# Kernel optimization log

Measured on AMD Instinct MI355X. Metric: run time of the kernel, lower is better.

Reference implementation:

```python
import jax, jax.numpy as jnp
import numpy as np

B, S, D, H = 2, 4096, 512, 8
HD = D // H

def setup_inputs() -> dict:
    key = jax.random.key(0)
    ks = jax.random.split(key, 9)
    s = 1.0 / np.sqrt(D)
    inp = {"x": jax.random.normal(ks[0], (B, S, D), dtype=jnp.float32)}
    names = ["Wq", "Wk", "Wv", "Wo"]
    for i, n in enumerate(names):
        inp[n] = jax.random.uniform(ks[1 + 2 * i], (D, D), jnp.float32, -s, s)
        inp["b" + n[1]] = jax.random.uniform(ks[2 + 2 * i], (D,), jnp.float32, -s, s)
    return inp


def reference(x, Wq, bq, Wk, bk, Wv, bv, Wo, bo):
    # projections (torch Linear: x @ W.T + b)
    def proj(W, b):
        return (x @ W.T + b).reshape(B, S, H, HD).transpose(0, 2, 1, 3)  # [B,H,S,HD]
    q = proj(Wq, bq)
    k = proj(Wk, bk)
    v = proj(Wv, bv)
    scores = jnp.einsum("bhqd,bhkd->bhqk", q, k) / np.sqrt(HD).astype(np.float32)
    attn = jax.nn.softmax(scores, axis=-1)
    out = jnp.einsum("bhqk,bhkd->bhqd", attn, v)
    out = out.transpose(0, 2, 1, 3).reshape(B, S, D)
    return out @ Wo.T + bo
```

## Files before the change

kernel.cpp:

```cpp
#include <hip/hip_runtime.h>
#include <hip/hip_bf16.h>

#define DEV __device__ __forceinline__

typedef float f32x4 __attribute__((ext_vector_type(4)));
typedef float f32x16 __attribute__((ext_vector_type(16)));
typedef __bf16 bf16x8 __attribute__((ext_vector_type(8)));
typedef unsigned short u16;
typedef unsigned short u16x8 __attribute__((ext_vector_type(8)));

DEV u16 f2bf(float f) {
    __bf16 h = (__bf16)f;
    return __builtin_bit_cast(u16, h);
}
DEV float bf2f(u16 u) {
    __bf16 h = __builtin_bit_cast(__bf16, u);
    return (float)h;
}

DEV f32x4 mfma16(bf16x8 a, bf16x8 b, f32x4 c) {
    return __builtin_amdgcn_mfma_f32_16x16x32_bf16(a, b, c, 0, 0, 0);
}
DEV f32x16 mfma32(bf16x8 a, bf16x8 b, f32x16 c) {
    return __builtin_amdgcn_mfma_f32_32x32x16_bf16(a, b, c, 0, 0, 0);
}

DEV unsigned cvtpk(float lo, float hi) {
    unsigned r;
    asm("v_cvt_pk_bf16_f32 %0, %1, %2" : "=v"(r) : "v"(lo), "v"(hi));
    return r;
}
DEV void pswap(unsigned& a, unsigned& b) {
    asm volatile("v_permlane32_swap_b32 %0, %1" : "+v"(a), "+v"(b));
}

DEV void gll16(const u16* g, u16* l) {
    __builtin_amdgcn_global_load_lds(
        (const __attribute__((address_space(1))) unsigned int*)g,
        (__attribute__((address_space(3))) unsigned int*)l,
        16, 0, 0);
}

DEV int kidx(int row, int col) { return row * 64 + (col ^ ((row & 7) << 3)); }
DEV int xidx(int row, int col) { return row * 32 + (col ^ ((row & 3) << 3)); }

__global__ __launch_bounds__(256) void cvt_kernel(
    const float* __restrict__ x, const float* __restrict__ wq,
    const float* __restrict__ wk, const float* __restrict__ wv,
    const float* __restrict__ wo,
    u16* __restrict__ xb, u16* __restrict__ wb)
{
    size_t e0 = ((size_t)blockIdx.x * 256 + threadIdx.x) * 8;
    const float* src; u16* dst; size_t off;
    if (e0 < 4194304) { src = x; dst = xb; off = e0; }
    else {
        size_t r = e0 - 4194304;
        int seg = (int)(r >> 18);
        src = (seg == 0) ? wq : (seg == 1) ? wk : (seg == 2) ? wv : wo;
        dst = wb + (size_t)seg * 262144;
        off = r & 262143;
    }
    f32x4 a = *(const f32x4*)(src + off);
    f32x4 b = *(const f32x4*)(src + off + 4);
    u16x8 o;
    #pragma unroll
    for (int i = 0; i < 4; ++i) { o[i] = f2bf(a[i]); o[i + 4] = f2bf(b[i]); }
    *(u16x8*)(dst + off) = o;
}

__global__ __launch_bounds__(256) void proj_qkv_kernel(
    const u16* __restrict__ xb, const u16* __restrict__ wb,
    const float* __restrict__ bq, const float* __restrict__ bk, const float* __restrict__ bv,
    u16* __restrict__ qo, u16* __restrict__ ko, u16* __restrict__ vo)
{
    __shared__ u16 Xs[2][128 * 32], Wsh[2][128 * 32];
    const int tid = threadIdx.x;
    const int m0 = blockIdx.x * 128, n0 = blockIdx.y * 128, z = blockIdx.z;
    const u16* W = wb + (size_t)z * 262144;
    const float* bias = (z == 0) ? bq : (z == 1) ? bk : bv;

    const int lane = tid & 63, wv = tid >> 6;
    const int g = lane >> 4, c = lane & 15;
    const int wr = wv >> 1, wcl = wv & 1;

    const int r0 = wv * 32 + (lane >> 2);
    const int csz = (((lane & 3) ^ ((lane >> 2) & 3)) << 3);
    const u16* xg0 = xb + (size_t)(m0 + r0) * 512 + csz;
    const u16* xg1 = xg0 + 16 * 512;
    const u16* wg0 = W + (size_t)(n0 + r0) * 512 + csz;
    const u16* wg1 = wg0 + 16 * 512;

    f32x4 acc[4][4] = {};

    gll16(xg0, &Xs[0][wv * 1024]);
    gll16(xg1, &Xs[0][wv * 1024 + 512]);
    gll16(wg0, &Wsh[0][wv * 1024]);
    gll16(wg1, &Wsh[0][wv * 1024 + 512]);

    for (int it = 0; it < 16; ++it) {
        const int p = it & 1;
        __syncthreads();
        if (it < 15) {
            const int kn = (it + 1) * 32;
            gll16(xg0 + kn, &Xs[p ^ 1][wv * 1024]);
            gll16(xg1 + kn, &Xs[p ^ 1][wv * 1024 + 512]);
            gll16(wg0 + kn, &Wsh[p ^ 1][wv * 1024]);
            gll16(wg1 + kn, &Wsh[p ^ 1][wv * 1024 + 512]);
        }

        bf16x8 af[4], bfr[4];
        #pragma unroll
        for (int mt = 0; mt < 4; ++mt)
            af[mt] = *(const bf16x8*)&Xs[p][xidx(wr * 64 + mt * 16 + c, g * 8)];
        #pragma unroll
        for (int nt = 0; nt < 4; ++nt)
            bfr[nt] = *(const bf16x8*)&Wsh[p][xidx(wcl * 64 + nt * 16 + c, g * 8)];

        if (z < 2) {
            #pragma unroll
            for (int mt = 0; mt < 4; ++mt)
                #pragma unroll
                for (int nt = 0; nt < 4; ++nt)
                    acc[mt][nt] = mfma16(af[mt], bfr[nt], acc[mt][nt]);
        } else {
            #pragma unroll
            for (int mt = 0; mt < 4; ++mt)
                #pragma unroll
                for (int nt = 0; nt < 4; ++nt)
                    acc[mt][nt] = mfma16(bfr[nt], af[mt], acc[mt][nt]);
        }
    }

    if (z < 2) {
        const float scale = (z == 0) ? 0.18033688011112042f : 1.0f;
        u16* outp = (z == 0) ? qo : ko;
        float bn[4];
        #pragma unroll
        for (int nt = 0; nt < 4; ++nt) bn[nt] = bias[n0 + wcl * 64 + nt * 16 + c];
        #pragma unroll
        for (int mt = 0; mt < 4; ++mt)
            #pragma unroll
            for (int r = 0; r < 4; ++r) {
                int mg = m0 + wr * 64 + mt * 16 + g * 4 + r;
                int b = mg >> 12, s = mg & 4095;
                #pragma unroll
                for (int nt = 0; nt < 4; ++nt) {
                    int ng = n0 + wcl * 64 + nt * 16 + c;
                    int h = ng >> 6, d = ng & 63;
                    outp[((size_t)(b * 8 + h) * 4096 + s) * 64 + d] =
                        f2bf((acc[mt][nt][r] + bn[nt]) * scale);
                }
            }
    } else {
        #pragma unroll
        for (int nt = 0; nt < 4; ++nt)
            #pragma unroll
            for (int r = 0; r < 4; ++r) {
                int ng = n0 + wcl * 64 + nt * 16 + g * 4 + r;
                int h = ng >> 6, d = ng & 63;
                float bnr = bias[ng];
                #pragma unroll
                for (int mt = 0; mt < 4; ++mt) {
                    int mg = m0 + wr * 64 + mt * 16 + c;
                    int b = mg >> 12, s = mg & 4095;
                    vo[((size_t)(b * 8 + h) * 64 + d) * 4096 + s] =
                        f2bf(acc[mt][nt][r] + bnr);
                }
            }
    }
}

__global__ __launch_bounds__(256, 4) void flash_attn_kernel(
    const u16* __restrict__ Q, const u16* __restrict__ K,
    const u16* __restrict__ Vt, u16* __restrict__ Opart, float* __restrict__ lbuf)
{
    __shared__ u16 Ks[2][64 * 64];
    __shared__ u16 Vs[2][64 * 64];

    const int tid = threadIdx.x;
    const int bh = blockIdx.y;
    const int q0 = blockIdx.x * 128;
    const int half = blockIdx.z;
    const int kvbase = half * 2048;
    const int lane = tid & 63, wv = tid >> 6;
    const int l31 = lane & 31, hi = lane >> 5;

    const u16* Qb = Q  + (size_t)bh * (4096 * 64);
    const u16* Kb = K  + (size_t)bh * (4096 * 64);
    const u16* Vb = Vt + (size_t)bh * (64 * 4096);

    u16x8 onesu;
    #pragma unroll
    for (int i = 0; i < 8; ++i) onesu[i] = 0x3F80;
    const bf16x8 ones = __builtin_bit_cast(bf16x8, onesu);

    const int qrow = q0 + wv * 32 + l31;
    bf16x8 qf[4];
    #pragma unroll
    for (int ds = 0; ds < 4; ++ds)
        qf[ds] = *(const bf16x8*)(Qb + (size_t)qrow * 64 + ds * 16 + hi * 8);

    f32x16 oA[2] = {};
    f32x16 oL = {};

    const int kr = wv * 16 + (lane >> 3);
    const int csz = (((lane & 7) ^ (lane >> 3)) << 3);
    const u16* kg0 = Kb + (size_t)(kvbase + kr) * 64 + csz;
    const u16* kg1 = kg0 + 8 * 64;
    const u16* vg0 = Vb + (size_t)kr * 4096 + kvbase + csz;
    const u16* vg1 = vg0 + 8 * 4096;

    gll16(kg0, &Ks[0][wv * 1024]);
    gll16(kg1, &Ks[0][wv * 1024 + 512]);
    gll16(vg0, &Vs[0][wv * 1024]);
    gll16(vg1, &Vs[0][wv * 1024 + 512]);

    for (int t = 0; t < 32; ++t) {
        const int p = t & 1;
        __syncthreads();
        if (t < 31) {
            const size_t ko = (size_t)(t + 1) * 4096;
            const size_t vofs = (size_t)(t + 1) * 64;
            gll16(kg0 + ko, &Ks[p ^ 1][wv * 1024]);
            gll16(kg1 + ko, &Ks[p ^ 1][wv * 1024 + 512]);
            gll16(vg0 + vofs, &Vs[p ^ 1][wv * 1024]);
            gll16(vg1 + vofs, &Vs[p ^ 1][wv * 1024 + 512]);
        }

        #pragma unroll
        for (int ct = 0; ct < 2; ++ct) {
            f32x16 sA = {};
            __builtin_amdgcn_s_setprio(1);
            #pragma unroll
            for (int ds = 0; ds < 4; ++ds) {
                bf16x8 kf = *(const bf16x8*)&Ks[p][kidx(ct * 32 + l31, ds * 16 + hi * 8)];
                sA = mfma32(kf, qf[ds], sA);
            }
            __builtin_amdgcn_s_setprio(0);

            float pv[16];
            #pragma unroll
            for (int r = 0; r < 16; ++r)
                pv[r] = __builtin_amdgcn_exp2f(sA[r]);

            unsigned a0 = cvtpk(pv[0],  pv[1]),  a1 = cvtpk(pv[2],  pv[3]);
            unsigned b0 = cvtpk(pv[4],  pv[5]),  b1 = cvtpk(pv[6],  pv[7]);
            pswap(a0, b0); pswap(a1, b1);
            uint4 w0; w0.x = a0; w0.y = a1; w0.z = b0; w0.w = b1;
            bf16x8 pfa = __builtin_bit_cast(bf16x8, w0);
            unsigned c0 = cvtpk(pv[8],  pv[9]),  c1 = cvtpk(pv[10], pv[11]);
            unsigned d0 = cvtpk(pv[12], pv[13]), d1 = cvtpk(pv[14], pv[15]);
            pswap(c0, d0); pswap(c1, d1);
            uint4 w1; w1.x = c0; w1.y = c1; w1.z = d0; w1.w = d1;
            bf16x8 pfb = __builtin_bit_cast(bf16x8, w1);

            __builtin_amdgcn_s_setprio(1);
            oL = mfma32(ones, pfa, oL);
            oL = mfma32(ones, pfb, oL);
            #pragma unroll
            for (int hf = 0; hf < 2; ++hf) {
                const int ks = 2 * ct + hf;
                const bf16x8 pfx = hf ? pfb : pfa;
                bf16x8 vf0 = *(const bf16x8*)&Vs[p][kidx(l31,      ks * 16 + hi * 8)];
                bf16x8 vf1 = *(const bf16x8*)&Vs[p][kidx(32 + l31, ks * 16 + hi * 8)];
                oA[0] = mfma32(vf0, pfx, oA[0]);
                oA[1] = mfma32(vf1, pfx, oA[1]);
            }
            __builtin_amdgcn_s_setprio(0);
        }
    }

    if (hi == 0)
        lbuf[(size_t)(half * 16 + bh) * 4096 + qrow] = oL[0];

    const int b = bh >> 3, h = bh & 7;
    u16* Ob = Opart + (size_t)half * 4194304 +
              ((size_t)(b * 4096 + qrow)) * 512 + h * 64;
    #pragma unroll
    for (int dt = 0; dt < 2; ++dt) {
        const f32x16 oa = dt ? oA[1] : oA[0];
        #pragma unroll
        for (int qd = 0; qd < 4; ++qd) {
            unsigned w0 = cvtpk(oa[qd * 4 + 0], oa[qd * 4 + 1]);
            unsigned w1 = cvtpk(oa[qd * 4 + 2], oa[qd * 4 + 3]);
            uint2 st; st.x = w0; st.y = w1;
            *(uint2*)(Ob + dt * 32 + qd * 8 + hi * 4) = st;
        }
    }
}

__global__ __launch_bounds__(256) void combine_kernel(
    const u16* __restrict__ Opart, const float* __restrict__ lbuf,
    u16* __restrict__ obuf)
{
    const size_t idx8 = ((size_t)blockIdx.x * 256 + threadIdx.x) * 8;
    const int m = (int)(idx8 >> 9);
    const int hd = (int)(idx8 & 511);
    const int b = m >> 12, s = m & 4095, h = hd >> 6;
    const int bh = b * 8 + h;
    const float la = lbuf[(size_t)bh * 4096 + s];
    const float lb = lbuf[(size_t)(16 + bh) * 4096 + s];
    const float inv = 1.0f / (la + lb);
    u16x8 a = *(const u16x8*)(Opart + idx8);
    u16x8 c = *(const u16x8*)(Opart + 4194304 + idx8);
    u16x8 o;
    #pragma unroll
    for (int i = 0; i < 8; ++i)
        o[i] = f2bf((bf2f(a[i]) + bf2f(c[i])) * inv);
    *(u16x8*)(obuf + idx8) = o;
}

__global__ __launch_bounds__(256) void out_proj_kernel(
    const u16* __restrict__ Ob, const u16* __restrict__ Wob,
    const float* __restrict__ bo, float* __restrict__ out)
{
    __shared__ u16 Xs[2][128 * 32], Wsh[2][128 * 32];
    const int tid = threadIdx.x;
    const int m0 = blockIdx.x * 128, n0 = blockIdx.y * 128;

    const int lane = tid & 63, wv = tid >> 6;
    const int g = lane >> 4, c = lane & 15;
    const int wr = wv >> 1, wcl = wv & 1;

    const int r0 = wv * 32 + (lane >> 2);
    const int csz = (((lane & 3) ^ ((lane >> 2) & 3)) << 3);
    const u16* xg0 = Ob + (size_t)(m0 + r0) * 512 + csz;
    const u16* xg1 = xg0 + 16 * 512;
    const u16* wg0 = Wob + (size_t)(n0 + r0) * 512 + csz;
    const u16* wg1 = wg0 + 16 * 512;

    f32x4 acc[4][4] = {};

    gll16(xg0, &Xs[0][wv * 1024]);
    gll16(xg1, &Xs[0][wv * 1024 + 512]);
    gll16(wg0, &Wsh[0][wv * 1024]);
    gll16(wg1, &Wsh[0][wv * 1024 + 512]);

    for (int it = 0; it < 16; ++it) {
        const int p = it & 1;
        __syncthreads();
        if (it < 15) {
            const int kn = (it + 1) * 32;
            gll16(xg0 + kn, &Xs[p ^ 1][wv * 1024]);
            gll16(xg1 + kn, &Xs[p ^ 1][wv * 1024 + 512]);
            gll16(wg0 + kn, &Wsh[p ^ 1][wv * 1024]);
            gll16(wg1 + kn, &Wsh[p ^ 1][wv * 1024 + 512]);
        }

        bf16x8 af[4], bfr[4];
        #pragma unroll
        for (int mt = 0; mt < 4; ++mt)
            af[mt] = *(const bf16x8*)&Xs[p][xidx(wr * 64 + mt * 16 + c, g * 8)];
        #pragma unroll
        for (int nt = 0; nt < 4; ++nt)
            bfr[nt] = *(const bf16x8*)&Wsh[p][xidx(wcl * 64 + nt * 16 + c, g * 8)];

        #pragma unroll
        for (int mt = 0; mt < 4; ++mt)
            #pragma unroll
            for (int nt = 0; nt < 4; ++nt)
                acc[mt][nt] = mfma16(bfr[nt], af[mt], acc[mt][nt]);
    }

    #pragma unroll
    for (int nt = 0; nt < 4; ++nt) {
        f32x4 bi = *(const f32x4*)&bo[n0 + wcl * 64 + nt * 16 + g * 4];
        #pragma unroll
        for (int mt = 0; mt < 4; ++mt) {
            int m = m0 + wr * 64 + mt * 16 + c;
            f32x4 v;
            #pragma unroll
            for (int r = 0; r < 4; ++r) v[r] = acc[mt][nt][r] + bi[r];
            *(f32x4*)&out[(size_t)m * 512 + n0 + wcl * 64 + nt * 16 + g * 4] = v;
        }
    }
}

extern "C" void kernel_launch(void* const* d_in, const int* in_sizes, int n_in,
                              void* d_out, int out_size, void* d_ws, size_t ws_size,
                              hipStream_t stream) {
    const float* x  = (const float*)d_in[0];
    const float* Wq = (const float*)d_in[1];
    const float* bq = (const float*)d_in[2];
    const float* Wk = (const float*)d_in[3];
    const float* bk = (const float*)d_in[4];
    const float* Wv = (const float*)d_in[5];
    const float* bv = (const float*)d_in[6];
    const float* Wo = (const float*)d_in[7];
    const float* bo = (const float*)d_in[8];
    float* out = (float*)d_out;

    const size_t NQKV = (size_t)2 * 8 * 4096 * 64;
    u16* qw = (u16*)d_ws;
    u16* kw = qw + NQKV;
    u16* vw = kw + NQKV;
    u16* wbuf = vw + NQKV;
    float* lbuf = (float*)(wbuf + 4 * 262144);
    u16* xbuf = (u16*)(lbuf + 2 * 16 * 4096);
    u16* opart = (u16*)d_out;
    u16* obuf = qw;

    cvt_kernel<<<2560, 256, 0, stream>>>(x, Wq, Wk, Wv, Wo, xbuf, wbuf);
    proj_qkv_kernel<<<dim3(64, 4, 3), 256, 0, stream>>>(xbuf, wbuf, bq, bk, bv, qw, kw, vw);
    flash_attn_kernel<<<dim3(32, 16, 2), 256, 0, stream>>>(qw, kw, vw, opart, lbuf);
    combine_kernel<<<2048, 256, 0, stream>>>(opart, lbuf, obuf);
    out_proj_kernel<<<dim3(64, 4), 256, 0, stream>>>(obuf, wbuf + 3 * 262144, bo, out);
}
```

Measured before the change: 140.2 us.

## Split KV within block across waves and merge in LDS, dropping combine kernel

The flash attention kernel now processes 64 query rows per block, with two wave pairs each handling half of every 64-key tile, instead of splitting the KV range across two grid blocks. The partial outputs and row sums are merged through shared memory at the end, and the result is written normalized directly. This removes the separate combine kernel and the bf16 partial-output round trip through global memory. In exchange each wave does half the compute per tile, so per-tile sync and load overhead is amortized over less math, and there is an extra LDS exchange at the end.

Result: no change. 140.5 us (+0.2%).

```diff
diff --git a/kernel.cpp b/kernel.cpp
--- a/kernel.cpp
+++ b/kernel.cpp
@@ -12,10 +12,6 @@
 DEV u16 f2bf(float f) {
     __bf16 h = (__bf16)f;
     return __builtin_bit_cast(u16, h);
-}
-DEV float bf2f(u16 u) {
-    __bf16 h = __builtin_bit_cast(__bf16, u);
-    return (float)h;
 }
 
 DEV f32x4 mfma16(bf16x8 a, bf16x8 b, f32x4 c) {
@@ -172,18 +168,16 @@
 
 __global__ __launch_bounds__(256, 4) void flash_attn_kernel(
     const u16* __restrict__ Q, const u16* __restrict__ K,
-    const u16* __restrict__ Vt, u16* __restrict__ Opart, float* __restrict__ lbuf)
+    const u16* __restrict__ Vt, u16* __restrict__ obuf)
 {
-    __shared__ u16 Ks[2][64 * 64];
-    __shared__ u16 Vs[2][64 * 64];
+    __shared__ u16 smem[16384];
 
     const int tid = threadIdx.x;
     const int bh = blockIdx.y;
-    const int q0 = blockIdx.x * 128;
-    const int half = blockIdx.z;
-    const int kvbase = half * 2048;
+    const int q0 = blockIdx.x * 64;
     const int lane = tid & 63, wv = tid >> 6;
     const int l31 = lane & 31, hi = lane >> 5;
+    const int qi = wv >> 1, ki = wv & 1;
 
     const u16* Qb = Q  + (size_t)bh * (4096 * 64);
     const u16* Kb = K  + (size_t)bh * (4096 * 64);
@@ -194,7 +188,7 @@
     for (int i = 0; i < 8; ++i) onesu[i] = 0x3F80;
     const bf16x8 ones = __builtin_bit_cast(bf16x8, onesu);
 
-    const int qrow = q0 + wv * 32 + l31;
+    const int qrow = q0 + qi * 32 + l31;
     bf16x8 qf[4];
     #pragma unroll
     for (int ds = 0; ds < 4; ++ds)
@@ -205,109 +199,101 @@
 
     const int kr = wv * 16 + (lane >> 3);
     const int csz = (((lane & 7) ^ (lane >> 3)) << 3);
-    const u16* kg0 = Kb + (size_t)(kvbase + kr) * 64 + csz;
+    const u16* kg0 = Kb + (size_t)kr * 64 + csz;
     const u16* kg1 = kg0 + 8 * 64;
-    const u16* vg0 = Vb + (size_t)kr * 4096 + kvbase + csz;
+    const u16* vg0 = Vb + (size_t)kr * 4096 + csz;
     const u16* vg1 = vg0 + 8 * 4096;
 
-    gll16(kg0, &Ks[0][wv * 1024]);
-    gll16(kg1, &Ks[0][wv * 1024 + 512]);
-    gll16(vg0, &Vs[0][wv * 1024]);
-    gll16(vg1, &Vs[0][wv * 1024 + 512]);
-
-    for (int t = 0; t < 32; ++t) {
+    gll16(kg0, &smem[wv * 1024]);
+    gll16(kg1, &smem[wv * 1024 + 512]);
+    gll16(vg0, &smem[8192 + wv * 1024]);
+    gll16(vg1, &smem[8192 + wv * 1024 + 512]);
+
+    for (int t = 0; t < 64; ++t) {
         const int p = t & 1;
+        const u16* Ksp = smem + p * 4096;
+        const u16* Vsp = smem + 8192 + p * 4096;
         __syncthreads();
-        if (t < 31) {
+        if (t < 63) {
             const size_t ko = (size_t)(t + 1) * 4096;
             const size_t vofs = (size_t)(t + 1) * 64;
-            gll16(kg0 + ko, &Ks[p ^ 1][wv * 1024]);
-            gll16(kg1 + ko, &Ks[p ^ 1][wv * 1024 + 512]);
-            gll16(vg0 + vofs, &Vs[p ^ 1][wv * 1024]);
-            gll16(vg1 + vofs, &Vs[p ^ 1][wv * 1024 + 512]);
-        }
-
-        #pragma unroll
-        for (int ct = 0; ct < 2; ++ct) {
-            f32x16 sA = {};
-            __builtin_amdgcn_s_setprio(1);
-            #pragma unroll
-            for (int ds = 0; ds < 4; ++ds) {
-                bf16x8 kf = *(const bf16x8*)&Ks[p][kidx(ct * 32 + l31, ds * 16 + hi * 8)];
-                sA = mfma32(kf, qf[ds], sA);
+            u16* Kn = smem + (p ^ 1) * 4096;
+            u16* Vn = smem + 8192 + (p ^ 1) * 4096;
+            gll16(kg0 + ko, &Kn[wv * 1024]);
+            gll16(kg1 + ko, &Kn[wv * 1024 + 512]);
+            gll16(vg0 + vofs, &Vn[wv * 1024]);
+            gll16(vg1 + vofs, &Vn[wv * 1024 + 512]);
+        }
+
+        f32x16 sA = {};
+        __builtin_amdgcn_s_setprio(1);
+        #pragma unroll
+        for (int ds = 0; ds < 4; ++ds) {
+            bf16x8 kf = *(const bf16x8*)&Ksp[kidx(ki * 32 + l31, ds * 16 + hi * 8)];
+            sA = mfma32(kf, qf[ds], sA);
+        }
+        __builtin_amdgcn_s_setprio(0);
+
+        float pv[16];
+        #pragma unroll
+        for (int r = 0; r < 16; ++r)
+            pv[r] = __builtin_amdgcn_exp2f(sA[r]);
+
+        unsigned a0 = cvtpk(pv[0],  pv[1]),  a1 = cvtpk(pv[2],  pv[3]);
+        unsigned b0 = cvtpk(pv[4],  pv[5]),  b1 = cvtpk(pv[6],  pv[7]);
+        pswap(a0, b0); pswap(a1, b1);
+        uint4 w0; w0.x = a0; w0.y = a1; w0.z = b0; w0.w = b1;
+        bf16x8 pfa = __builtin_bit_cast(bf16x8, w0);
+        unsigned c0 = cvtpk(pv[8],  pv[9]),  c1 = cvtpk(pv[10], pv[11]);
+        unsigned d0 = cvtpk(pv[12], pv[13]), d1 = cvtpk(pv[14], pv[15]);
+        pswap(c0, d0); pswap(c1, d1);
+        uint4 w1; w1.x = c0; w1.y = c1; w1.z = d0; w1.w = d1;
+        bf16x8 pfb = __builtin_bit_cast(bf16x8, w1);
+
+        __builtin_amdgcn_s_setprio(1);
+        oL = mfma32(ones, pfa, oL);
+        oL = mfma32(ones, pfb, oL);
+        #pragma unroll
+        for (int hf = 0; hf < 2; ++hf) {
+            const int ks = 2 * ki + hf;
+            const bf16x8 pfx = hf ? pfb : pfa;
+            bf16x8 vf0 = *(const bf16x8*)&Vsp[kidx(l31,      ks * 16 + hi * 8)];
+            bf16x8 vf1 = *(const bf16x8*)&Vsp[kidx(32 + l31, ks * 16 + hi * 8)];
+            oA[0] = mfma32(vf0, pfx, oA[0]);
+            oA[1] = mfma32(vf1, pfx, oA[1]);
+        }
+        __builtin_amdgcn_s_setprio(0);
+    }
+
+    __syncthreads();
+    float* xch = (float*)smem;
+    if (ki) {
+        float* dst = xch + ((size_t)qi * 64 + lane) * 33;
+        #pragma unroll
+        for (int i = 0; i < 16; ++i) dst[i] = oA[0][i];
+        #pragma unroll
+        for (int i = 0; i < 16; ++i) dst[16 + i] = oA[1][i];
+        dst[32] = oL[0];
+    }
+    __syncthreads();
+    if (!ki) {
+        const float* src = xch + ((size_t)qi * 64 + lane) * 33;
+        const float inv = 1.0f / (oL[0] + src[32]);
+        const int b = bh >> 3, h = bh & 7;
+        u16* Ob = obuf + ((size_t)(b * 4096 + qrow)) * 512 + h * 64;
+        #pragma unroll
+        for (int dt = 0; dt < 2; ++dt) {
+            #pragma unroll
+            for (int qd = 0; qd < 4; ++qd) {
+                float v0 = (oA[dt][qd * 4 + 0] + src[dt * 16 + qd * 4 + 0]) * inv;
+                float v1 = (oA[dt][qd * 4 + 1] + src[dt * 16 + qd * 4 + 1]) * inv;
+                float v2 = (oA[dt][qd * 4 + 2] + src[dt * 16 + qd * 4 + 2]) * inv;
+                float v3 = (oA[dt][qd * 4 + 3] + src[dt * 16 + qd * 4 + 3]) * inv;
+                uint2 st; st.x = cvtpk(v0, v1); st.y = cvtpk(v2, v3);
+                *(uint2*)(Ob + dt * 32 + qd * 8 + hi * 4) = st;
             }
-            __builtin_amdgcn_s_setprio(0);
-
-            float pv[16];
-            #pragma unroll
-            for (int r = 0; r < 16; ++r)
-                pv[r] = __builtin_amdgcn_exp2f(sA[r]);
-
-            unsigned a0 = cvtpk(pv[0],  pv[1]),  a1 = cvtpk(pv[2],  pv[3]);
-            unsigned b0 = cvtpk(pv[4],  pv[5]),  b1 = cvtpk(pv[6],  pv[7]);
-            pswap(a0, b0); pswap(a1, b1);
-            uint4 w0; w0.x = a0; w0.y = a1; w0.z = b0; w0.w = b1;
-            bf16x8 pfa = __builtin_bit_cast(bf16x8, w0);
-            unsigned c0 = cvtpk(pv[8],  pv[9]),  c1 = cvtpk(pv[10], pv[11]);
-            unsigned d0 = cvtpk(pv[12], pv[13]), d1 = cvtpk(pv[14], pv[15]);
-            pswap(c0, d0); pswap(c1, d1);
-            uint4 w1; w1.x = c0; w1.y = c1; w1.z = d0; w1.w = d1;
-            bf16x8 pfb = __builtin_bit_cast(bf16x8, w1);
-
-            __builtin_amdgcn_s_setprio(1);
-            oL = mfma32(ones, pfa, oL);
-            oL = mfma32(ones, pfb, oL);
-            #pragma unroll
-            for (int hf = 0; hf < 2; ++hf) {
-                const int ks = 2 * ct + hf;
-                const bf16x8 pfx = hf ? pfb : pfa;
-                bf16x8 vf0 = *(const bf16x8*)&Vs[p][kidx(l31,      ks * 16 + hi * 8)];
-                bf16x8 vf1 = *(const bf16x8*)&Vs[p][kidx(32 + l31, ks * 16 + hi * 8)];
-                oA[0] = mfma32(vf0, pfx, oA[0]);
-                oA[1] = mfma32(vf1, pfx, oA[1]);
-            }
-            __builtin_amdgcn_s_setprio(0);
-        }
-    }
-
-    if (hi == 0)
-        lbuf[(size_t)(half * 16 + bh) * 4096 + qrow] = oL[0];
-
-    const int b = bh >> 3, h = bh & 7;
-    u16* Ob = Opart + (size_t)half * 4194304 +
-              ((size_t)(b * 4096 + qrow)) * 512 + h * 64;
-    #pragma unroll
-    for (int dt = 0; dt < 2; ++dt) {
-        const f32x16 oa = dt ? oA[1] : oA[0];
-        #pragma unroll
-        for (int qd = 0; qd < 4; ++qd) {
-            unsigned w0 = cvtpk(oa[qd * 4 + 0], oa[qd * 4 + 1]);
-            unsigned w1 = cvtpk(oa[qd * 4 + 2], oa[qd * 4 + 3]);
-            uint2 st; st.x = w0; st.y = w1;
-            *(uint2*)(Ob + dt * 32 + qd * 8 + hi * 4) = st;
-        }
-    }
-}
-
-__global__ __launch_bounds__(256) void combine_kernel(
-    const u16* __restrict__ Opart, const float* __restrict__ lbuf,
-    u16* __restrict__ obuf)
-{
-    const size_t idx8 = ((size_t)blockIdx.x * 256 + threadIdx.x) * 8;
-    const int m = (int)(idx8 >> 9);
-    const int hd = (int)(idx8 & 511);
-    const int b = m >> 12, s = m & 4095, h = hd >> 6;
-    const int bh = b * 8 + h;
-    const float la = lbuf[(size_t)bh * 4096 + s];
-    const float lb = lbuf[(size_t)(16 + bh) * 4096 + s];
-    const float inv = 1.0f / (la + lb);
-    u16x8 a = *(const u16x8*)(Opart + idx8);
-    u16x8 c = *(const u16x8*)(Opart + 4194304 + idx8);
-    u16x8 o;
-    #pragma unroll
-    for (int i = 0; i < 8; ++i)
-        o[i] = f2bf((bf2f(a[i]) + bf2f(c[i])) * inv);
-    *(u16x8*)(obuf + idx8) = o;
+        }
+    }
 }
 
 __global__ __launch_bounds__(256) void out_proj_kernel(
@@ -395,14 +381,11 @@
     u16* kw = qw + NQKV;
     u16* vw = kw + NQKV;
     u16* wbuf = vw + NQKV;
-    float* lbuf = (float*)(wbuf + 4 * 262144);
-    u16* xbuf = (u16*)(lbuf + 2 * 16 * 4096);
-    u16* opart = (u16*)d_out;
-    u16* obuf = qw;
+    u16* xbuf = wbuf + 4 * 262144;
+    u16* obuf = xbuf;
 
     cvt_kernel<<<2560, 256, 0, stream>>>(x, Wq, Wk, Wv, Wo, xbuf, wbuf);
     proj_qkv_kernel<<<dim3(64, 4, 3), 256, 0, stream>>>(xbuf, wbuf, bq, bk, bv, qw, kw, vw);
-    flash_attn_kernel<<<dim3(32, 16, 2), 256, 0, stream>>>(qw, kw, vw, opart, lbuf);
-    combine_kernel<<<2048, 256, 0, stream>>>(opart, lbuf, obuf);
+    flash_attn_kernel<<<dim3(64, 16), 256, 0, stream>>>(qw, kw, vw, obuf);
     out_proj_kernel<<<dim3(64, 4), 256, 0, stream>>>(obuf, wbuf + 3 * 262144, bo, out);
 }
```
